# Optimization experiments

Hardware: AMD Instinct MI355X
Metric: run time of the kernel (lower is better)

Reference implementation:

```python
import jax, jax.numpy as jnp
import numpy as np

N = 100_000      # nodes per batched graph
E = 1_600_000    # edges
IN = 128         # in_channels_node
H = 64           # hidden_dim
R = 32           # num_relations
B = 512          # graphs in batch


def setup_inputs() -> dict:
    key = jax.random.key(0)
    ks = jax.random.split(key, 32)
    def w(k, shape, fan_in):
        return jax.random.normal(k, shape, jnp.float32) / np.float32(np.sqrt(fan_in))
    inp = {}
    inp["state_x"] = jax.random.normal(ks[0], (N, IN), jnp.float32)
    inp["state_edge_index"] = jax.random.randint(ks[1], (2, E), 0, N, dtype=jnp.int32)
    inp["state_edge_type"] = jax.random.randint(ks[2], (E,), 0, R, dtype=jnp.int32)
    inp["state_batch"] = jnp.sort(jax.random.randint(ks[3], (N,), 0, B, dtype=jnp.int32))
    inp["goal_x"] = jax.random.normal(ks[4], (N, IN), jnp.float32)
    inp["goal_edge_index"] = jax.random.randint(ks[5], (2, E), 0, N, dtype=jnp.int32)
    inp["goal_edge_type"] = jax.random.randint(ks[6], (E,), 0, R, dtype=jnp.int32)
    inp["goal_batch"] = jnp.sort(jax.random.randint(ks[7], (N,), 0, B, dtype=jnp.int32))
    inp["depth"] = jax.random.normal(ks[8], (B,), jnp.float32)
    # RGCN params: per-relation weights [R,in,out], root weight [in,out], bias [out]
    inp["sW1"], inp["sRoot1"], inp["sB1"] = w(ks[9], (R, IN, H), IN), w(ks[10], (IN, H), IN), jnp.zeros((H,), jnp.float32)
    inp["sW2"], inp["sRoot2"], inp["sB2"] = w(ks[11], (R, H, H), H), w(ks[12], (H, H), H), jnp.zeros((H,), jnp.float32)
    inp["gW1"], inp["gRoot1"], inp["gB1"] = w(ks[13], (R, IN, H), IN), w(ks[14], (IN, H), IN), jnp.zeros((H,), jnp.float32)
    inp["gW2"], inp["gRoot2"], inp["gB2"] = w(ks[15], (R, H, H), H), w(ks[16], (H, H), H), jnp.zeros((H,), jnp.float32)
    inp["rW1"], inp["rB1"] = w(ks[17], (2 * H + 1, H), 2 * H + 1), jnp.zeros((H,), jnp.float32)
    inp["rW2"], inp["rB2"] = w(ks[18], (H, 1), H), jnp.zeros((1,), jnp.float32)
    return inp


def rgcn_conv(x, src, dst, edge_type, W, Wroot, b):
    """PyG RGCNConv: out_i = x_i@Wroot + b + sum_r mean_{j in N_r(i)} x_j@W_r."""
    n = x.shape[0]
    out_dim = W.shape[2]

    def body(acc, r):
        mask = (edge_type == r)
        xr = x @ W[r]                                   # [N, out]
        msg = jnp.where(mask[:, None], xr[src], 0.0)    # [E, out]
        s = jax.ops.segment_sum(msg, dst, num_segments=n)
        cnt = jax.ops.segment_sum(mask.astype(x.dtype), dst, num_segments=n)
        return acc + s / jnp.maximum(cnt, 1.0)[:, None], None

    acc, _ = jax.lax.scan(body, jnp.zeros((n, out_dim), x.dtype),
                          jnp.arange(W.shape[0]))
    return acc + x @ Wroot + b


def encode(x, edge_index, edge_type, batch, W1, Wr1, b1, W2, Wr2, b2, num_graphs):
    src, dst = edge_index[0], edge_index[1]
    h = jax.nn.relu(rgcn_conv(x, src, dst, edge_type, W1, Wr1, b1))
    h = jax.nn.relu(rgcn_conv(h, src, dst, edge_type, W2, Wr2, b2))
    s = jax.ops.segment_sum(h, batch, num_segments=num_graphs)
    cnt = jax.ops.segment_sum(jnp.ones((x.shape[0],), x.dtype), batch,
                              num_segments=num_graphs)
    return s / jnp.maximum(cnt, 1.0)[:, None]        # global_mean_pool


def reference(state_x, state_edge_index, state_edge_type, state_batch,
              goal_x, goal_edge_index, goal_edge_type, goal_batch, depth,
              sW1, sRoot1, sB1, sW2, sRoot2, sB2,
              gW1, gRoot1, gB1, gW2, gRoot2, gB2,
              rW1, rB1, rW2, rB2):
    num_graphs = depth.shape[0]
    state_emb = encode(state_x, state_edge_index, state_edge_type, state_batch,
                       sW1, sRoot1, sB1, sW2, sRoot2, sB2, num_graphs)
    goal_emb = encode(goal_x, goal_edge_index, goal_edge_type, goal_batch,
                      gW1, gRoot1, gB1, gW2, gRoot2, gB2, num_graphs)
    graph_emb = jnp.concatenate([state_emb, goal_emb], axis=1)  # [B, 2H]
    d = depth.reshape(-1, 1)
    d = (d - d.mean()) / (jnp.std(d) + 1e-6)
    z = jnp.concatenate([graph_emb, d], axis=1)                 # [B, 2H+1]
    pred = (jax.nn.relu(z @ rW1 + rB1) @ rW2 + rB2).squeeze(1)  # [B]
    return pred
```

## Files before the change

kernel.cpp:

```cpp
#include <hip/hip_runtime.h>

constexpr int HD     = 64;
constexpr int RNUM   = 32;
constexpr int STRIDE = 256;
constexpr int CAPE   = 280;

typedef __attribute__((ext_vector_type(4))) float f32x4;
typedef __attribute__((ext_vector_type(8))) short bf16x8;

#define WS_ALIGN(x) (((x) + size_t(255)) & ~size_t(255))

__device__ inline float b2f(unsigned short u) {
    return __uint_as_float(((unsigned)u) << 16);
}
__device__ inline unsigned short f2b(float f) {
    unsigned u = __float_as_uint(f);
    u = (u + 0x7FFF + ((u >> 16) & 1)) >> 16;
    return (unsigned short)u;
}
__device__ inline unsigned pack2bf(float a, float b) {
    return (unsigned)f2b(a) | ((unsigned)f2b(b) << 16);
}


__global__ __launch_bounds__(256) void count_kernel(
    const int* __restrict__ dst, int* __restrict__ deg, int* __restrict__ rank, int E)
{
    int e = blockIdx.x * 256 + threadIdx.x;
    if (e < E) rank[e] = atomicAdd(&deg[dst[e]], 1);
}

__global__ __launch_bounds__(256) void scan1_kernel(
    const int* __restrict__ in, int* __restrict__ out, int* __restrict__ part, int n)
{
    __shared__ int ls[256];
    const int i0 = blockIdx.x * 1024 + threadIdx.x * 4;
    int v[4];
    int tot = 0;
#pragma unroll
    for (int u = 0; u < 4; ++u) {
        int x = (i0 + u < n) ? in[i0 + u] : 0;
        v[u] = tot;
        tot += x;
    }
    ls[threadIdx.x] = tot;
    __syncthreads();
    for (int off = 1; off < 256; off <<= 1) {
        int x = (threadIdx.x >= off) ? ls[threadIdx.x - off] : 0;
        __syncthreads();
        ls[threadIdx.x] += x;
        __syncthreads();
    }
    int texcl = ls[threadIdx.x] - tot;
#pragma unroll
    for (int u = 0; u < 4; ++u)
        if (i0 + u < n) out[i0 + u] = texcl + v[u];
    if (threadIdx.x == 255) part[blockIdx.x] = ls[255];
}

__global__ void scan2_kernel(int* __restrict__ part, int nb, int* __restrict__ out, int n)
{
    if (threadIdx.x == 0) {
        int acc = 0;
        for (int i = 0; i < nb; ++i) { int t = part[i]; part[i] = acc; acc += t; }
        out[n] = acc;
    }
}

__global__ __launch_bounds__(256) void scan3_kernel(
    int* __restrict__ out, const int* __restrict__ part, int n)
{
    int i = blockIdx.x * 256 + threadIdx.x;
    if (i < n) out[i] += part[blockIdx.x >> 2];
}

__global__ __launch_bounds__(256) void boundary_kernel(
    const int* __restrict__ nstart, int* __restrict__ bstart, int N, int nblk)
{
    int b = blockIdx.x * 256 + threadIdx.x;
    if (b > nblk) return;
    if (b == nblk) { bstart[b] = N; return; }
    int target = b * STRIDE;
    int lo = 0, hi = N;
    while (lo < hi) {
        int mid = (lo + hi) >> 1;
        if (nstart[mid] < target) lo = mid + 1; else hi = mid;
    }
    bstart[b] = lo;
}

__global__ __launch_bounds__(256) void scatter_kernel(
    const int* __restrict__ src, const int* __restrict__ dst, const int* __restrict__ et,
    const int* __restrict__ rank, const int* __restrict__ nstart,
    int* __restrict__ es, int E)
{
    int e = blockIdx.x * 256 + threadIdx.x;
    if (e < E)
        es[nstart[dst[e]] + rank[e]] = src[e] | (et[e] << 17);
}

__global__ __launch_bounds__(256) void tobf16_kernel(
    const float* __restrict__ in, unsigned short* __restrict__ out, int total8)
{
    int i = blockIdx.x * 256 + threadIdx.x;
    if (i >= total8) return;
    const float4* ip = (const float4*)(in + (size_t)i * 8);
    float4 a = ip[0], b = ip[1];
    uint4 o;
    o.x = pack2bf(a.x, a.y); o.y = pack2bf(a.z, a.w);
    o.z = pack2bf(b.x, b.y); o.w = pack2bf(b.z, b.w);
    *(uint4*)(out + (size_t)i * 8) = o;
}

template<int K>
__global__ __launch_bounds__(256) void wfrag_kernel(
    const float* __restrict__ W, unsigned short* __restrict__ wfrag)
{
    constexpr int KS = K / 32;
    int idx = blockIdx.x * 256 + threadIdx.x;
    int total = RNUM * KS * 4 * 64;
    if (idx >= total) return;
    int lane = idx & 63;
    int tmp = idx >> 6;
    int jt = tmp & 3; tmp >>= 2;
    int ks = tmp % KS;
    int t = tmp / KS;
    int col = jt * 16 + (lane & 15);
    int kb = ks * 32 + (lane >> 4) * 8;
    const float* Wp = W + ((size_t)t * K + kb) * HD + col;
    uint4 o;
    o.x = pack2bf(Wp[0 * HD], Wp[1 * HD]);
    o.y = pack2bf(Wp[2 * HD], Wp[3 * HD]);
    o.z = pack2bf(Wp[4 * HD], Wp[5 * HD]);
    o.w = pack2bf(Wp[6 * HD], Wp[7 * HD]);
    *(uint4*)(wfrag + (size_t)idx * 8) = o;
}

template<int K>
__global__ __launch_bounds__(256) void wfroot_kernel(
    const float* __restrict__ Root, unsigned short* __restrict__ wfr)
{
    constexpr int KS = K / 32;
    int idx = blockIdx.x * 256 + threadIdx.x;
    int total = KS * 4 * 64;
    if (idx >= total) return;
    int lane = idx & 63;
    int tmp = idx >> 6;
    int jt = tmp & 3;
    int ks = tmp >> 2;
    int col = jt * 16 + (lane & 15);
    int kb = ks * 32 + (lane >> 4) * 8;
    const float* Wp = Root + (size_t)kb * HD + col;
    uint4 o;
    o.x = pack2bf(Wp[0 * HD], Wp[1 * HD]);
    o.y = pack2bf(Wp[2 * HD], Wp[3 * HD]);
    o.z = pack2bf(Wp[4 * HD], Wp[5 * HD]);
    o.w = pack2bf(Wp[6 * HD], Wp[7 * HD]);
    *(uint4*)(wfr + (size_t)idx * 8) = o;
}

template<int K>
__global__ __launch_bounds__(256) void rootmm_kernel(
    const unsigned short* __restrict__ xb, const unsigned short* __restrict__ wfr,
    const float* __restrict__ bias, unsigned short* __restrict__ hroot, int N)
{
    constexpr int KS = K / 32;
    __shared__ unsigned short sW[KS * 4 * 64 * 8];
    __shared__ float sbias[HD];
    const int tid = threadIdx.x;
    for (int i = tid; i < KS * 256; i += 256)
        ((uint4*)sW)[i] = ((const uint4*)wfr)[i];
    if (tid < HD) sbias[tid] = bias[tid];
    __syncthreads();
    const int lane = tid & 63;
    const int wid = tid >> 6;
    const int jb = (lane >> 4) * 4;
#pragma unroll
    for (int b = 0; b < 4; ++b) {
        const int node = blockIdx.x * 256 + wid * 64 + b * 16 + (lane & 15);
        const int nclamp = node < N ? node : N - 1;
        const unsigned short* xp = xb + (size_t)nclamp * K + (lane >> 4) * 8;
        f32x4 acc[4];
#pragma unroll
        for (int jt = 0; jt < 4; ++jt) acc[jt] = (f32x4)0.0f;
#pragma unroll
        for (int ks = 0; ks < KS; ++ks) {
            bf16x8 bx = *(const bf16x8*)(xp + ks * 32);
#pragma unroll
            for (int jt = 0; jt < 4; ++jt) {
                bf16x8 aw = *(const bf16x8*)(sW + (size_t)((ks * 4 + jt) * 64 + lane) * 8);
                acc[jt] = __builtin_amdgcn_mfma_f32_16x16x32_bf16(aw, bx, acc[jt], 0, 0, 0);
            }
        }
        if (node < N) {
            unsigned short* hr = hroot + (size_t)node * HD + jb;
#pragma unroll
            for (int jt = 0; jt < 4; ++jt) {
                const int j0 = jt * 16 + jb;
                uint2 pk;
                pk.x = pack2bf(acc[jt][0] + sbias[j0 + 0], acc[jt][1] + sbias[j0 + 1]);
                pk.y = pack2bf(acc[jt][2] + sbias[j0 + 2], acc[jt][3] + sbias[j0 + 3]);
                *(uint2*)(hr + jt * 16) = pk;
            }
        }
    }
}

template<int K>
__global__ __launch_bounds__(256) void fused_kernel(
    const unsigned short* __restrict__ xb, const int* __restrict__ es,
    const int* __restrict__ nstart, const int* __restrict__ bstart,
    const unsigned short* __restrict__ wfrag,
    const unsigned short* __restrict__ hroot,
    unsigned short* __restrict__ hout)
{
    constexpr int KS = K / 32;
    __shared__ unsigned short msg[CAPE * HD];
    __shared__ int s_es[CAPE];
    __shared__ unsigned short s_idx[CAPE];
    __shared__ unsigned short s_pos[CAPE];
    __shared__ int hist[RNUM], tbase[RNUM], tcur[RNUM];
    __shared__ int bdesc[CAPE / 16 + RNUM + 2];
    __shared__ int nb_s, nend_s;
    __shared__ int scnt[4][RNUM];
    __shared__ float sinv[4][RNUM];

    const int tid = threadIdx.x, lane = tid & 63, wid = tid >> 6;
    int n0 = bstart[blockIdx.x];
    const int n1 = bstart[blockIdx.x + 1];

    while (n0 < n1) {
        if (wid == 0) {
            const int ea_ = nstart[n0];
            int m = n0;
            for (;;) {
                int cand = m + 1 + lane;
                bool ok = (cand <= n1) && (nstart[cand] - ea_ <= CAPE);
                unsigned long long mm = __ballot(ok);
                int f = (~mm == 0ULL) ? 64 : (__ffsll((unsigned long long)(~mm)) - 1);
                m += f;
                if (f < 64 || m >= n1) break;
            }
            if (m == n0) m = n0 + 1;
            if (m > n1) m = n1;
            if (lane == 0) nend_s = m;
        }
        __syncthreads();
        const int na = n0, ne = nend_s;
        const int ea = nstart[na];
        int cnt = nstart[ne] - ea;
        if (cnt > CAPE) cnt = CAPE;

        for (int i = tid; i < cnt; i += 256) s_es[i] = es[ea + i];
        if (tid < RNUM) hist[tid] = 0;
        __syncthreads();
        for (int i = tid; i < cnt; i += 256)
            atomicAdd(&hist[(s_es[i] >> 17) & 31], 1);
        __syncthreads();
        if (wid == 0) {
            const int t = lane & 31;
            int h = (lane < RNUM) ? hist[t] : 0;
            int nbatch = (h + 15) >> 4;
            int ph = h, pb = nbatch;
            for (int off = 1; off < 32; off <<= 1) {
                int vh = __shfl_up(ph, off, 32);
                int vb = __shfl_up(pb, off, 32);
                if ((lane & 31) >= off) { ph += vh; pb += vb; }
            }
            if (lane < RNUM) {
                const int tb = ph - h;
                tbase[t] = tb;
                int bo = pb - nbatch;
                for (int c2 = 0; c2 < h; c2 += 16)
                    bdesc[bo++] = (t << 10) | (tb + c2);
                if (t == RNUM - 1) nb_s = pb;
            }
        }
        __syncthreads();
        if (tid < RNUM) tcur[tid] = tbase[tid];
        __syncthreads();
        for (int i = tid; i < cnt; i += 256) {
            int t = (s_es[i] >> 17) & 31;
            int pos = atomicAdd(&tcur[t], 1);
            s_idx[pos] = (unsigned short)i;
            s_pos[i] = (unsigned short)pos;
        }
        __syncthreads();

        {
            const int nbt = nb_s;
            const int b0 = (nbt * wid) >> 2;
            const int b1 = (nbt * (wid + 1)) >> 2;
            if (b0 < b1) {
                int c_c;
                bool val_c;
                const unsigned short* wt_c;
                bf16x8 bx_c[KS];
                {
                    const int desc = bdesc[b0];
                    const int t = desc >> 10;
                    const int p0 = desc & 1023;
                    const int tend = tbase[t] + hist[t];
                    c_c = p0 + (lane & 15);
                    val_c = c_c < tend;
                    wt_c = wfrag + (size_t)t * (KS * 2048);
                    const int idx = s_idx[val_c ? c_c : p0];
                    const unsigned short* xp =
                        xb + (size_t)(s_es[idx] & 0x1FFFF) * K + (lane >> 4) * 8;
#pragma unroll
                    for (int ks = 0; ks < KS; ++ks) bx_c[ks] = *(const bf16x8*)(xp + ks * 32);
                }
                for (int bi = b0; bi < b1; ++bi) {
                    int c_n = 0;
                    bool val_n = false;
                    const unsigned short* wt_n = wt_c;
                    bf16x8 bx_n[KS];
                    if (bi + 1 < b1) {
                        const int desc = bdesc[bi + 1];
                        const int t = desc >> 10;
                        const int p0 = desc & 1023;
                        const int tend = tbase[t] + hist[t];
                        c_n = p0 + (lane & 15);
                        val_n = c_n < tend;
                        wt_n = wfrag + (size_t)t * (KS * 2048);
                        const int idx = s_idx[val_n ? c_n : p0];
                        const unsigned short* xp =
                            xb + (size_t)(s_es[idx] & 0x1FFFF) * K + (lane >> 4) * 8;
#pragma unroll
                        for (int ks = 0; ks < KS; ++ks) bx_n[ks] = *(const bf16x8*)(xp + ks * 32);
                    }
                    f32x4 acc[4];
#pragma unroll
                    for (int jt = 0; jt < 4; ++jt) acc[jt] = (f32x4)0.0f;
#pragma unroll
                    for (int ks = 0; ks < KS; ++ks) {
#pragma unroll
                        for (int jt = 0; jt < 4; ++jt) {
                            bf16x8 aw = *(const bf16x8*)(wt_c + (size_t)((ks * 4 + jt) * 64 + lane) * 8);
                            acc[jt] = __builtin_amdgcn_mfma_f32_16x16x32_bf16(aw, bx_c[ks], acc[jt], 0, 0, 0);
                        }
                    }
                    if (val_c) {
                        char* mr = (char*)(msg + c_c * HD);
                        const int swz = (c_c & 7) << 4;
#pragma unroll
                        for (int jt = 0; jt < 4; ++jt) {
                            uint2 pk;
                            pk.x = pack2bf(acc[jt][0], acc[jt][1]);
                            pk.y = pack2bf(acc[jt][2], acc[jt][3]);
                            *(uint2*)(mr + (((lane >> 4) * 8 + jt * 32) ^ swz)) = pk;
                        }
                    }
                    c_c = c_n; val_c = val_n; wt_c = wt_n;
#pragma unroll
                    for (int ks = 0; ks < KS; ++ks) bx_c[ks] = bx_n[ks];
                }
            }
        }
        __syncthreads();

        for (int n = na + wid; n < ne; n += 4) {
            const int rs = nstart[n] - ea;
            int re = nstart[n + 1] - ea;
            if (re > cnt) re = cnt;
            if (lane < RNUM) scnt[wid][lane] = 0;
            for (int e = rs + lane; e < re; e += 64)
                atomicAdd(&scnt[wid][(s_es[e] >> 17) & 31], 1);
            if (lane < RNUM) {
                int c = scnt[wid][lane];
                sinv[wid][lane] = 1.0f / (float)(c > 1 ? c : 1);
            }
            float acc = b2f(hroot[(size_t)n * HD + lane]);
            for (int e = rs; e < re; ++e) {
                const float iv = sinv[wid][(s_es[e] >> 17) & 31];
                const int row = s_pos[e];
                const char* mr = (const char*)(msg + row * HD);
                acc += iv * b2f(*(const unsigned short*)(mr + ((lane * 2) ^ ((row & 7) << 4))));
            }
            hout[(size_t)n * HD + lane] = f2b(fmaxf(acc, 0.f));
        }
        __syncthreads();
        n0 = ne;
    }
}

__global__ __launch_bounds__(256) void pool_kernel(
    const unsigned short* __restrict__ h, const int* __restrict__ batch,
    float* __restrict__ pool, float* __restrict__ gcnt, int col0, int n)
{
    const int lane = threadIdx.x & 63;
    const int wid = (blockIdx.x * 256 + threadIdx.x) >> 6;
    const int RANGE = 256;
    int n0 = wid * RANGE;
    if (n0 >= n) return;
    int n1 = n0 + RANGE;
    if (n1 > n) n1 = n;
    int cur = batch[n0];
    float acc = 0.f, c = 0.f;
    for (int i = n0; i < n1; ++i) {
        int b = batch[i];
        if (b != cur) {
            unsafeAtomicAdd(&pool[(size_t)cur * 128 + col0 + lane], acc);
            if (lane == 0) unsafeAtomicAdd(&gcnt[cur], c);
            acc = 0.f; c = 0.f; cur = b;
        }
        acc += b2f(h[(size_t)i * HD + lane]);
        c += 1.f;
    }
    unsafeAtomicAdd(&pool[(size_t)cur * 128 + col0 + lane], acc);
    if (lane == 0) unsafeAtomicAdd(&gcnt[cur], c);
}

__global__ __launch_bounds__(512) void depth_kernel(
    const float* __restrict__ depth, float* __restrict__ dnorm, int Bn)
{
    __shared__ float ls[8];
    __shared__ float smean, sstd;
    const int t = threadIdx.x, lane = t & 63, wv = t >> 6;
    float d = (t < Bn) ? depth[t] : 0.f;
    float s = d;
#pragma unroll
    for (int o = 32; o; o >>= 1) s += __shfl_down(s, o, 64);
    if (lane == 0) ls[wv] = s;
    __syncthreads();
    if (t == 0) {
        float tot = 0.f;
        for (int i = 0; i < 8; ++i) tot += ls[i];
        smean = tot / (float)Bn;
    }
    __syncthreads();
    float mean = smean;
    float df = (t < Bn) ? (d - mean) : 0.f;
    s = df * df;
#pragma unroll
    for (int o = 32; o; o >>= 1) s += __shfl_down(s, o, 64);
    __syncthreads();
    if (lane == 0) ls[wv] = s;
    __syncthreads();
    if (t == 0) {
        float tot = 0.f;
        for (int i = 0; i < 8; ++i) tot += ls[i];
        sstd = sqrtf(tot / (float)Bn);
    }
    __syncthreads();
    if (t < Bn) dnorm[t] = df / (sstd + 1e-6f);
}

__global__ __launch_bounds__(256) void regress_kernel(
    const float* __restrict__ pool, const float* __restrict__ gcnt_s,
    const float* __restrict__ gcnt_g, const float* __restrict__ dnorm,
    const float* __restrict__ rW1, const float* __restrict__ rB1,
    const float* __restrict__ rW2, const float* __restrict__ rB2,
    float* __restrict__ pred, int Bn)
{
    const int lane = threadIdx.x & 63;
    const int g = (blockIdx.x * 256 + threadIdx.x) >> 6;
    if (g >= Bn) return;
    const float is = 1.f / fmaxf(gcnt_s[g], 1.f);
    const float ig = 1.f / fmaxf(gcnt_g[g], 1.f);
    const float* pr = pool + (size_t)g * 128;
    float acc = rB1[lane];
    for (int k = 0; k < 64; ++k)
        acc = fmaf(pr[k] * is, rW1[k * 64 + lane], acc);
    for (int k = 64; k < 128; ++k)
        acc = fmaf(pr[k] * ig, rW1[k * 64 + lane], acc);
    acc = fmaf(dnorm[g], rW1[128 * 64 + lane], acc);
    float v = fmaxf(acc, 0.f) * rW2[lane];
#pragma unroll
    for (int o = 32; o; o >>= 1) v += __shfl_down(v, o, 64);
    if (lane == 0) pred[g] = v + rB2[0];
}


extern "C" void kernel_launch(void* const* d_in, const int* in_sizes, int n_in,
                              void* d_out, int out_size, void* d_ws, size_t ws_size,
                              hipStream_t stream)
{
    const int E1 = in_sizes[2];
    const int E2 = in_sizes[6];
    const int Emax = E1 > E2 ? E1 : E2;
    const int N = in_sizes[3];
    const int IN = in_sizes[0] / N;
    const int Bn = in_sizes[8];

    const float* state_x = (const float*)d_in[0];
    const int* s_ei = (const int*)d_in[1];
    const int* s_et = (const int*)d_in[2];
    const int* s_batch = (const int*)d_in[3];
    const float* goal_x = (const float*)d_in[4];
    const int* g_ei = (const int*)d_in[5];
    const int* g_et = (const int*)d_in[6];
    const int* g_batch = (const int*)d_in[7];
    const float* depth = (const float*)d_in[8];
    const float* sW1 = (const float*)d_in[9];
    const float* sRoot1 = (const float*)d_in[10];
    const float* sB1 = (const float*)d_in[11];
    const float* sW2 = (const float*)d_in[12];
    const float* sRoot2 = (const float*)d_in[13];
    const float* sB2 = (const float*)d_in[14];
    const float* gW1 = (const float*)d_in[15];
    const float* gRoot1 = (const float*)d_in[16];
    const float* gB1 = (const float*)d_in[17];
    const float* gW2 = (const float*)d_in[18];
    const float* gRoot2 = (const float*)d_in[19];
    const float* gB2 = (const float*)d_in[20];
    const float* rW1 = (const float*)d_in[21];
    const float* rB1 = (const float*)d_in[22];
    const float* rW2 = (const float*)d_in[23];
    const float* rB2 = (const float*)d_in[24];
    float* pred = (float*)d_out;

    const int nbScan = (N + 1023) / 1024;
    const int nblkMax = (Emax + STRIDE - 1) / STRIDE;

    char* p = (char*)d_ws;
    auto alloc = [&](size_t bytes) { char* r = p; p += WS_ALIGN(bytes); return r; };
    int* deg    = (int*)alloc((size_t)N * 4);
    int* nstart = (int*)alloc((size_t)(N + 1) * 4);
    int* rank   = (int*)alloc((size_t)Emax * 4);
    int* part   = (int*)alloc((size_t)nbScan * 4);
    int* bstart = (int*)alloc((size_t)(nblkMax + 1) * 4);
    int* es     = (int*)alloc((size_t)Emax * 4);
    unsigned short* xb    = (unsigned short*)alloc((size_t)N * IN * 2);
    unsigned short* h1    = (unsigned short*)alloc((size_t)N * HD * 2);
    unsigned short* h2    = (unsigned short*)alloc((size_t)N * HD * 2);
    unsigned short* hroot = (unsigned short*)alloc((size_t)N * HD * 2);
    unsigned short* wf1   = (unsigned short*)alloc((size_t)RNUM * 4 * 4 * 64 * 8 * 2);
    unsigned short* wf2   = (unsigned short*)alloc((size_t)RNUM * 2 * 4 * 64 * 8 * 2);
    unsigned short* wfr1  = (unsigned short*)alloc((size_t)4 * 4 * 64 * 8 * 2);
    unsigned short* wfr2  = (unsigned short*)alloc((size_t)2 * 4 * 64 * 8 * 2);
    float* pool   = (float*)alloc((size_t)Bn * 128 * 4);
    float* gcnt_s = (float*)alloc((size_t)Bn * 4);
    float* gcnt_g = (float*)alloc((size_t)Bn * 4);
    float* dnorm  = (float*)alloc((size_t)Bn * 4);

    hipMemsetAsync(pool, 0, (size_t)Bn * 128 * 4, stream);
    hipMemsetAsync(gcnt_s, 0, (size_t)Bn * 4, stream);
    hipMemsetAsync(gcnt_g, 0, (size_t)Bn * 4, stream);

    const int nmmB = (N + 255) / 256;

    for (int enc = 0; enc < 2; ++enc) {
        const float* x = enc ? goal_x : state_x;
        const int* ei = enc ? g_ei : s_ei;
        const int* et = enc ? g_et : s_et;
        const int* batch = enc ? g_batch : s_batch;
        const float* W1 = enc ? gW1 : sW1;
        const float* Root1 = enc ? gRoot1 : sRoot1;
        const float* B1 = enc ? gB1 : sB1;
        const float* W2 = enc ? gW2 : sW2;
        const float* Root2 = enc ? gRoot2 : sRoot2;
        const float* B2 = enc ? gB2 : sB2;
        float* gcnt = enc ? gcnt_g : gcnt_s;
        const int E = enc ? E2 : E1;
        const int* srcp = ei;
        const int* dstp = ei + E;
        const int ebl = (E + 255) / 256;
        const int nblk = (E + STRIDE - 1) / STRIDE;

        hipMemsetAsync(deg, 0, (size_t)N * 4, stream);

        count_kernel<<<ebl, 256, 0, stream>>>(dstp, deg, rank, E);
        scan1_kernel<<<nbScan, 256, 0, stream>>>(deg, nstart, part, N);
        scan2_kernel<<<1, 64, 0, stream>>>(part, nbScan, nstart, N);
        scan3_kernel<<<nbScan * 4, 256, 0, stream>>>(nstart, part, N);
        boundary_kernel<<<(nblk + 1 + 255) / 256, 256, 0, stream>>>(nstart, bstart, N, nblk);
        scatter_kernel<<<ebl, 256, 0, stream>>>(srcp, dstp, et, rank, nstart, es, E);

        tobf16_kernel<<<(N * IN / 8 + 255) / 256, 256, 0, stream>>>(x, xb, N * IN / 8);
        wfrag_kernel<128><<<(RNUM * 4 * 4 * 64 + 255) / 256, 256, 0, stream>>>(W1, wf1);
        wfrag_kernel<64><<<(RNUM * 2 * 4 * 64 + 255) / 256, 256, 0, stream>>>(W2, wf2);
        wfroot_kernel<128><<<(4 * 4 * 64 + 255) / 256, 256, 0, stream>>>(Root1, wfr1);
        wfroot_kernel<64><<<(2 * 4 * 64 + 255) / 256, 256, 0, stream>>>(Root2, wfr2);

        rootmm_kernel<128><<<nmmB, 256, 0, stream>>>(xb, wfr1, B1, hroot, N);
        fused_kernel<128><<<nblk, 256, 0, stream>>>(xb, es, nstart, bstart, wf1, hroot, h1);
        rootmm_kernel<64><<<nmmB, 256, 0, stream>>>(h1, wfr2, B2, hroot, N);
        fused_kernel<64><<<nblk, 256, 0, stream>>>(h1, es, nstart, bstart, wf2, hroot, h2);

        int pwaves = (N + 255) / 256;
        pool_kernel<<<(pwaves * 64 + 255) / 256, 256, 0, stream>>>(
            h2, batch, pool, gcnt, enc * 64, N);
    }

    depth_kernel<<<1, 512, 0, stream>>>(depth, dnorm, Bn);
    regress_kernel<<<(Bn * 64 + 255) / 256, 256, 0, stream>>>(
        pool, gcnt_s, gcnt_g, dnorm, rW1, rB1, rW2, rB2, pred, Bn);
}
```

Baseline: 1.301 ms.

## Fuse global mean pooling into second RGCN layer and shrink edge tiles

The second-layer fused kernel now accumulates ReLU outputs straight into per-graph pool sums with atomics. This removes the separate pool kernel and the h2 write and reread. Each wave now handles a contiguous node range, so runs of nodes from the same graph can be reduced locally before the atomic. The edge tile stride and LDS capacity also drop from 256/280 to 200/216, which gives more blocks with less shared memory each, at the cost of more atomics at block boundaries.

```diff
diff --git a/kernel.cpp b/kernel.cpp
--- a/kernel.cpp
+++ b/kernel.cpp
@@ -2,8 +2,8 @@
 
 constexpr int HD     = 64;
 constexpr int RNUM   = 32;
-constexpr int STRIDE = 256;
-constexpr int CAPE   = 280;
+constexpr int STRIDE = 200;
+constexpr int CAPE   = 216;
 
 typedef __attribute__((ext_vector_type(4))) float f32x4;
 typedef __attribute__((ext_vector_type(8))) short bf16x8;
@@ -206,13 +206,15 @@
     }
 }
 
-template<int K>
+template<int K, int PL>
 __global__ __launch_bounds__(256) void fused_kernel(
     const unsigned short* __restrict__ xb, const int* __restrict__ es,
     const int* __restrict__ nstart, const int* __restrict__ bstart,
     const unsigned short* __restrict__ wfrag,
     const unsigned short* __restrict__ hroot,
-    unsigned short* __restrict__ hout)
+    unsigned short* __restrict__ hout,
+    const int* __restrict__ batch, float* __restrict__ pool,
+    float* __restrict__ gcnt, int col0)
 {
     constexpr int KS = K / 32;
     __shared__ unsigned short msg[CAPE * HD];
@@ -359,56 +361,69 @@
         }
         __syncthreads();
 
-        for (int n = na + wid; n < ne; n += 4) {
-            const int rs = nstart[n] - ea;
-            int re = nstart[n + 1] - ea;
-            if (re > cnt) re = cnt;
-            if (lane < RNUM) scnt[wid][lane] = 0;
-            for (int e = rs + lane; e < re; e += 64)
-                atomicAdd(&scnt[wid][(s_es[e] >> 17) & 31], 1);
-            if (lane < RNUM) {
-                int c = scnt[wid][lane];
-                sinv[wid][lane] = 1.0f / (float)(c > 1 ? c : 1);
-            }
-            float acc = b2f(hroot[(size_t)n * HD + lane]);
-            for (int e = rs; e < re; ++e) {
-                const float iv = sinv[wid][(s_es[e] >> 17) & 31];
-                const int row = s_pos[e];
-                const char* mr = (const char*)(msg + row * HD);
-                acc += iv * b2f(*(const unsigned short*)(mr + ((lane * 2) ^ ((row & 7) << 4))));
-            }
-            hout[(size_t)n * HD + lane] = f2b(fmaxf(acc, 0.f));
+        if (PL) {
+            const int NL = ne - na;
+            const int ns = na + (NL * wid) / 4;
+            const int nf = na + (NL * (wid + 1)) / 4;
+            if (ns < nf) {
+                int cur = batch[ns];
+                float pacc = 0.f, pc = 0.f;
+                for (int n = ns; n < nf; ++n) {
+                    const int rs = nstart[n] - ea;
+                    int re = nstart[n + 1] - ea;
+                    if (re > cnt) re = cnt;
+                    if (lane < RNUM) scnt[wid][lane] = 0;
+                    for (int e = rs + lane; e < re; e += 64)
+                        atomicAdd(&scnt[wid][(s_es[e] >> 17) & 31], 1);
+                    if (lane < RNUM) {
+                        int c = scnt[wid][lane];
+                        sinv[wid][lane] = 1.0f / (float)(c > 1 ? c : 1);
+                    }
+                    float acc = b2f(hroot[(size_t)n * HD + lane]);
+                    for (int e = rs; e < re; ++e) {
+                        const float iv = sinv[wid][(s_es[e] >> 17) & 31];
+                        const int row = s_pos[e];
+                        const char* mr = (const char*)(msg + row * HD);
+                        acc += iv * b2f(*(const unsigned short*)(mr + ((lane * 2) ^ ((row & 7) << 4))));
+                    }
+                    float rv = fmaxf(acc, 0.f);
+                    int b = batch[n];
+                    if (b != cur) {
+                        unsafeAtomicAdd(&pool[(size_t)cur * 128 + col0 + lane], pacc);
+                        if (lane == 0) unsafeAtomicAdd(&gcnt[cur], pc);
+                        pacc = 0.f; pc = 0.f; cur = b;
+                    }
+                    pacc += rv;
+                    pc += 1.f;
+                }
+                unsafeAtomicAdd(&pool[(size_t)cur * 128 + col0 + lane], pacc);
+                if (lane == 0) unsafeAtomicAdd(&gcnt[cur], pc);
+            }
+        } else {
+            for (int n = na + wid; n < ne; n += 4) {
+                const int rs = nstart[n] - ea;
+                int re = nstart[n + 1] - ea;
+                if (re > cnt) re = cnt;
+                if (lane < RNUM) scnt[wid][lane] = 0;
+                for (int e = rs + lane; e < re; e += 64)
+                    atomicAdd(&scnt[wid][(s_es[e] >> 17) & 31], 1);
+                if (lane < RNUM) {
+                    int c = scnt[wid][lane];
+                    sinv[wid][lane] = 1.0f / (float)(c > 1 ? c : 1);
+                }
+                float acc = b2f(hroot[(size_t)n * HD + lane]);
+                for (int e = rs; e < re; ++e) {
+                    const float iv = sinv[wid][(s_es[e] >> 17) & 31];
+                    const int row = s_pos[e];
+                    const char* mr = (const char*)(msg + row * HD);
+                    acc += iv * b2f(*(const unsigned short*)(mr + ((lane * 2) ^ ((row & 7) << 4))));
+                }
+                hout[(size_t)n * HD + lane] = f2b(fmaxf(acc, 0.f));
+            }
         }
         __syncthreads();
         n0 = ne;
     }
-}
-
-__global__ __launch_bounds__(256) void pool_kernel(
-    const unsigned short* __restrict__ h, const int* __restrict__ batch,
-    float* __restrict__ pool, float* __restrict__ gcnt, int col0, int n)
-{
-    const int lane = threadIdx.x & 63;
-    const int wid = (blockIdx.x * 256 + threadIdx.x) >> 6;
-    const int RANGE = 256;
-    int n0 = wid * RANGE;
-    if (n0 >= n) return;
-    int n1 = n0 + RANGE;
-    if (n1 > n) n1 = n;
-    int cur = batch[n0];
-    float acc = 0.f, c = 0.f;
-    for (int i = n0; i < n1; ++i) {
-        int b = batch[i];
-        if (b != cur) {
-            unsafeAtomicAdd(&pool[(size_t)cur * 128 + col0 + lane], acc);
-            if (lane == 0) unsafeAtomicAdd(&gcnt[cur], c);
-            acc = 0.f; c = 0.f; cur = b;
-        }
-        acc += b2f(h[(size_t)i * HD + lane]);
-        c += 1.f;
-    }
-    unsafeAtomicAdd(&pool[(size_t)cur * 128 + col0 + lane], acc);
-    if (lane == 0) unsafeAtomicAdd(&gcnt[cur], c);
 }
 
 __global__ __launch_bounds__(512) void depth_kernel(
@@ -523,7 +538,6 @@
     int* es     = (int*)alloc((size_t)Emax * 4);
     unsigned short* xb    = (unsigned short*)alloc((size_t)N * IN * 2);
     unsigned short* h1    = (unsigned short*)alloc((size_t)N * HD * 2);
-    unsigned short* h2    = (unsigned short*)alloc((size_t)N * HD * 2);
     unsigned short* hroot = (unsigned short*)alloc((size_t)N * HD * 2);
     unsigned short* wf1   = (unsigned short*)alloc((size_t)RNUM * 4 * 4 * 64 * 8 * 2);
     unsigned short* wf2   = (unsigned short*)alloc((size_t)RNUM * 2 * 4 * 64 * 8 * 2);
@@ -574,13 +588,11 @@
         wfroot_kernel<64><<<(2 * 4 * 64 + 255) / 256, 256, 0, stream>>>(Root2, wfr2);
 
         rootmm_kernel<128><<<nmmB, 256, 0, stream>>>(xb, wfr1, B1, hroot, N);
-        fused_kernel<128><<<nblk, 256, 0, stream>>>(xb, es, nstart, bstart, wf1, hroot, h1);
+        fused_kernel<128, 0><<<nblk, 256, 0, stream>>>(
+            xb, es, nstart, bstart, wf1, hroot, h1, nullptr, nullptr, nullptr, 0);
         rootmm_kernel<64><<<nmmB, 256, 0, stream>>>(h1, wfr2, B2, hroot, N);
-        fused_kernel<64><<<nblk, 256, 0, stream>>>(h1, es, nstart, bstart, wf2, hroot, h2);
-
-        int pwaves = (N + 255) / 256;
-        pool_kernel<<<(pwaves * 64 + 255) / 256, 256, 0, stream>>>(
-            h2, batch, pool, gcnt, enc * 64, N);
+        fused_kernel<64, 1><<<nblk, 256, 0, stream>>>(
+            h1, es, nstart, bstart, wf2, hroot, nullptr, batch, pool, gcnt, enc * 64);
     }
 
     depth_kernel<<<1, 512, 0, stream>>>(depth, dnorm, Bn);
```

After: 1.315 ms. No clear change (+1.1%).
